# Optimization experiments

Hardware: AMD Instinct MI355X
Metric: run time of the kernel (lower is better)

Reference implementation:

```python
import jax, jax.numpy as jnp
import numpy as np

B, T, E = 2, 2048, 1024
H, D = 16, 64          # num_heads, head_dim (v_head_dim == head_dim)


def setup_inputs() -> dict:
    key = jax.random.key(0)
    ks = jax.random.split(key, 10)
    s = lambda fan_in: 1.0 / np.sqrt(fan_in)
    inp = {
        "embed": jax.random.normal(ks[0], (B, T, E), dtype=jnp.float32),
        "mask": jax.random.randint(ks[1], (B, T, T), 0, 2) > 0,
        # Linear weights stored as [in, out] (y = x @ W + b)
        "Wq": jax.random.uniform(ks[2], (E, H * D), minval=-s(E), maxval=s(E)),
        "bq": jnp.zeros((H * D,), jnp.float32),
        "Wk": jax.random.uniform(ks[3], (E, H * D), minval=-s(E), maxval=s(E)),
        "bk": jnp.zeros((H * D,), jnp.float32),
        "Wv": jax.random.uniform(ks[4], (E, H * D), minval=-s(E), maxval=s(E)),
        "bv": jnp.zeros((H * D,), jnp.float32),
        "Wz": jax.random.uniform(ks[5], (H * D, E), minval=-s(H * D), maxval=s(H * D)),
        "bz": jnp.zeros((E,), jnp.float32),
    }
    return inp


def reference(embed, mask, Wq, bq, Wk, bk, Wv, bv, Wz, bz):
    # Self-attention: context = embed
    q = (embed @ Wq + bq).reshape(B, T, H, D)   # b t h d
    k = (embed @ Wk + bk).reshape(B, T, H, D)   # b T h d
    v = (embed @ Wv + bv).reshape(B, T, H, D)   # b T h d

    scale = D ** (-0.5)
    score = jnp.einsum('bthd,bThd->bhtT', q, k) * scale   # [b,h,t,T] materialized, as in source
    max_neg = -jnp.finfo(score.dtype).max
    score = jnp.where(mask[:, None, :, :], score, max_neg)
    norm_score = jax.nn.softmax(score, axis=-1)
    z = jnp.einsum('bhtT,bThd->bthd', norm_score, v)      # [b,t,h,d]
    flat_z = z.reshape(B, T, H * D)
    return flat_z @ Wz + bz
```

## Files before the change

### kernel.cpp

```cpp
#include <hip/hip_runtime.h>
#include <hip/hip_bf16.h>


typedef __bf16 bf8_t  __attribute__((ext_vector_type(8)));
typedef __bf16 bf4_t  __attribute__((ext_vector_type(4)));
typedef float  f4_t   __attribute__((ext_vector_type(4)));

constexpr int Bb = 2, Tt = 2048, Hh = 16, Dd = 64;

#define ASYNC16(g, l)                                                        \
    __builtin_amdgcn_global_load_lds(                                        \
        (const __attribute__((address_space(1))) void*)(g),                  \
        (__attribute__((address_space(3))) void*)(l), 16, 0, 0)

#if __has_builtin(__builtin_amdgcn_exp2f)
#define EXP2F(x) __builtin_amdgcn_exp2f(x)
#else
#define EXP2F(x) exp2f(x)
#endif

__global__ __launch_bounds__(256) void prep_kernel(
    const float* __restrict__ embed, const int* __restrict__ mask,
    const float* __restrict__ w0, const float* __restrict__ w1,
    const float* __restrict__ w2, const float* __restrict__ w3,
    __bf16* __restrict__ o0, __bf16* __restrict__ o1,
    __bf16* __restrict__ o2, __bf16* __restrict__ o3,
    __bf16* __restrict__ Eb, unsigned* __restrict__ Mbits)
{
    int z = blockIdx.x;
    if (z < 4096) {
        const float* in; __bf16* out;
        switch (z >> 10) {
            case 0: in = w0; out = o0; break;
            case 1: in = w1; out = o1; break;
            case 2: in = w2; out = o2; break;
            default: in = w3; out = o3; break;
        }
        int rem = z & 1023;
        int bx = (rem & 31) * 32;
        int by = (rem >> 5) * 32;
        __shared__ float t[32][33];
        int x  = threadIdx.x & 31;
        int y0 = threadIdx.x >> 5;
        #pragma unroll
        for (int i = 0; i < 4; i++) {
            int y = y0 + i * 8;
            t[y][x] = in[(size_t)(by + y) * 1024 + bx + x];
        }
        __syncthreads();
        #pragma unroll
        for (int i = 0; i < 4; i++) {
            int y = y0 + i * 8;
            out[(size_t)(bx + y) * 1024 + by + x] = (__bf16)t[x][y];
        }
    } else if (z < 5120) {
        size_t base = (size_t)(z - 4096) * 4096;
        #pragma unroll
        for (int j = 0; j < 4; j++) {
            size_t i = base + j * 1024 + threadIdx.x * 4;
            float4 v = *reinterpret_cast<const float4*>(embed + i);
            bf4_t o = {(__bf16)v.x, (__bf16)v.y, (__bf16)v.z, (__bf16)v.w};
            *reinterpret_cast<bf4_t*>(Eb + i) = o;
        }
    } else {
        size_t g = (size_t)(z - 5120) * 256 + threadIdx.x;
        const int* mp = mask + g * 32;
        unsigned v = 0;
        #pragma unroll
        for (int i = 0; i < 8; i++) {
            int4 m4 = *reinterpret_cast<const int4*>(mp + i * 4);
            if (m4.x) v |= 1u << (i * 4 + 0);
            if (m4.y) v |= 1u << (i * 4 + 1);
            if (m4.z) v |= 1u << (i * 4 + 2);
            if (m4.w) v |= 1u << (i * 4 + 3);
        }
        Mbits[g] = v;
    }
}

template <int TM, typename OutT>
__device__ __forceinline__ void gemm_body(const __bf16* __restrict__ A,
                                          const __bf16* __restrict__ Bt,
                                          const float* __restrict__ bias,
                                          OutT* __restrict__ out,
                                          int mode, float oscale, int bx, int by)
{
    constexpr int NI = TM / 32;
    alignas(16) __shared__ __bf16 As[TM * 64];
    alignas(16) __shared__ __bf16 Bs[128 * 64];

    int tid  = threadIdx.x;
    int lane = tid & 63;
    int quad = lane >> 4;
    int l16  = lane & 15;
    int wave = tid >> 6;
    int wm   = wave >> 1, wn = wave & 1;

    f4_t acc[NI][4];
    #pragma unroll
    for (int i = 0; i < NI; i++)
        #pragma unroll
        for (int j = 0; j < 4; j++)
            acc[i][j] = f4_t{0.f, 0.f, 0.f, 0.f};

    for (int kt = 0; kt < 1024; kt += 64) {
        #pragma unroll
        for (int i = 0; i < TM / 32; i++) {
            int c   = tid + 256 * i;
            int row = c >> 3, j = c & 7;
            ASYNC16(A + (size_t)(by * TM + row) * 1024 + kt + ((j ^ (row & 7)) * 8),
                    &As[c * 8]);
        }
        #pragma unroll
        for (int i = 0; i < 4; i++) {
            int c   = tid + 256 * i;
            int row = c >> 3, j = c & 7;
            ASYNC16(Bt + (size_t)(bx * 128 + row) * 1024 + kt + ((j ^ (row & 7)) * 8),
                    &Bs[c * 8]);
        }
        __syncthreads();

        bf8_t af[2][NI], bfr[2][4];
        #pragma unroll
        for (int c = 0; c < 2; c++) {
            #pragma unroll
            for (int im = 0; im < NI; im++) {
                int row = wm * (TM / 2) + im * 16 + l16;
                af[c][im] = *reinterpret_cast<const bf8_t*>(
                    &As[row * 64 + (((c * 4 + quad) ^ (row & 7)) * 8)]);
            }
            #pragma unroll
            for (int in_ = 0; in_ < 4; in_++) {
                int row = wn * 64 + in_ * 16 + l16;
                bfr[c][in_] = *reinterpret_cast<const bf8_t*>(
                    &Bs[row * 64 + (((c * 4 + quad) ^ (row & 7)) * 8)]);
            }
        }
        #pragma unroll
        for (int c = 0; c < 2; c++)
            #pragma unroll
            for (int im = 0; im < NI; im++)
                #pragma unroll
                for (int in_ = 0; in_ < 4; in_++)
                    acc[im][in_] = __builtin_amdgcn_mfma_f32_16x16x32_bf16(
                        af[c][im], bfr[c][in_], acc[im][in_], 0, 0, 0);
        __syncthreads();
    }

    #pragma unroll
    for (int im = 0; im < NI; im++) {
        #pragma unroll
        for (int in_ = 0; in_ < 4; in_++) {
            int gc  = bx * 128 + wn * 64 + in_ * 16 + l16;
            float bb = bias[gc];
            int gr0 = by * TM + wm * (TM / 2) + im * 16 + quad * 4;
            if (mode == 2) {
                int b = gr0 >> 11, t0 = gr0 & 2047;
                int h = gc >> 6,  d = gc & 63;
                bf4_t ov;
                #pragma unroll
                for (int r = 0; r < 4; r++)
                    ov[r] = (__bf16)(acc[im][in_][r] + bb);
                *reinterpret_cast<bf4_t*>(
                    (__bf16*)out + ((size_t)(b * Hh + h) * Dd + d) * Tt + t0) = ov;
            } else {
                #pragma unroll
                for (int r = 0; r < 4; r++) {
                    int gr  = gr0 + r;
                    float v = (acc[im][in_][r] + bb) * oscale;
                    size_t idx;
                    if (mode == 0) {
                        idx = (size_t)gr * 1024 + gc;
                    } else {
                        int b = gr >> 11, t = gr & 2047;
                        int h = gc >> 6,  d = gc & 63;
                        idx = ((size_t)(b * Hh + h) * Tt + t) * Dd + d;
                    }
                    out[idx] = (OutT)v;
                }
            }
        }
    }
}

__global__ __launch_bounds__(256) void gemm_qkv_kernel(
    const __bf16* __restrict__ A,
    const __bf16* __restrict__ WqT, const __bf16* __restrict__ WkT, const __bf16* __restrict__ WvT,
    const float* __restrict__ bq,  const float* __restrict__ bk,  const float* __restrict__ bv,
    __bf16* __restrict__ Qo, __bf16* __restrict__ Ko, __bf16* __restrict__ Vo)
{
    const __bf16* Bt; const float* bias; __bf16* out; int mode; float sc;
    if      (blockIdx.z == 0) { Bt = WqT; bias = bq; out = Qo; mode = 1; sc = 0.18033688011112042f; }
    else if (blockIdx.z == 1) { Bt = WkT; bias = bk; out = Ko; mode = 1; sc = 1.f; }
    else                      { Bt = WvT; bias = bv; out = Vo; mode = 2; sc = 1.f; }
    gemm_body<128, __bf16>(A, Bt, bias, out, mode, sc, blockIdx.x, blockIdx.y);
}

__global__ __launch_bounds__(256) void gemm_out_kernel(
    const __bf16* __restrict__ A, const __bf16* __restrict__ Bt,
    const float* __restrict__ bias, float* __restrict__ out)
{
    gemm_body<64, float>(A, Bt, bias, out, 0, 1.f, blockIdx.x, blockIdx.y);
}

__global__ __launch_bounds__(1024, 8) void flash_kernel(
    const __bf16* __restrict__ Qb, const __bf16* __restrict__ Kb,
    const __bf16* __restrict__ Vb, const unsigned* __restrict__ Mbits,
    __bf16* __restrict__ Zb)
{
    alignas(16) __shared__ char smem[51200];
    __bf16* Ks = (__bf16*)smem;
    __bf16* Vs = (__bf16*)(smem + 16384);
    __bf16* Ps = (__bf16*)(smem + 32768);
    float*  fscr = (float*)smem;

    int tid  = threadIdx.x;
    int lane = tid & 63;
    int wave = tid >> 6;
    int s    = wave >> 1;
    int hk   = wave & 1;
    int quad = lane >> 4;
    int l16  = lane & 15;
    int b = blockIdx.z, h = blockIdx.y;
    int bh = b * Hh + h;
    int qrow = blockIdx.x * 128 + s * 16;

    int st = tid & 511, srow = st >> 3, sj = st & 7;
    bool stageK = (wave < 8);
    const __bf16* kgp = Kb + ((size_t)bh * Tt + srow) * Dd + ((sj ^ (srow & 7)) * 8);
    const __bf16* vgp = Vb + ((size_t)bh * Dd + srow) * Tt + ((sj ^ (srow & 7)) * 8);
    const __bf16* sgp = stageK ? kgp : vgp;
    const size_t  sstep = stageK ? (size_t)64 * Dd : (size_t)64;
    __bf16* sdstp = (stageK ? Ks : Vs) + st * 8;

    bf8_t qf[2];
    #pragma unroll
    for (int c = 0; c < 2; c++)
        qf[c] = *reinterpret_cast<const bf8_t*>(
            Qb + ((size_t)bh * Tt + qrow + l16) * Dd + c * 32 + quad * 8);

    bf8_t ones;
    #pragma unroll
    for (int i = 0; i < 8; i++) ones[i] = (__bf16)1.0f;

    const unsigned* bmp = Mbits + ((size_t)b * Tt + qrow + l16) * 64;

    f4_t lacc = f4_t{0.f, 0.f, 0.f, 0.f};
    f4_t o[4];
    #pragma unroll
    for (int d = 0; d < 4; d++) o[d] = f4_t{0.f, 0.f, 0.f, 0.f};

    __bf16* pw = Ps + s * (16 * 72);

    bf8_t sreg = *reinterpret_cast<const bf8_t*>(sgp);
    unsigned long long mreg = *reinterpret_cast<const unsigned long long*>(bmp);

    for (int kt = 0; kt < Tt; kt += 64) {
        int par = (kt >> 6) & 1;
        *reinterpret_cast<bf8_t*>(sdstp + par * 4096) = sreg;
        unsigned nib0 = (unsigned)(mreg >> (hk * 32 + quad * 4)) & 0xFu;
        unsigned nib1 = (unsigned)(mreg >> (hk * 32 + 16 + quad * 4)) & 0xFu;
        __syncthreads();

        int ktn = (kt + 64 < Tt) ? kt + 64 : 0;
        sreg = *reinterpret_cast<const bf8_t*>(sgp + (size_t)(ktn >> 6) * sstep);
        mreg = *reinterpret_cast<const unsigned long long*>(bmp + (ktn >> 5));

        f4_t sA = f4_t{0.f, 0.f, 0.f, 0.f};
        f4_t sB = f4_t{0.f, 0.f, 0.f, 0.f};
        __builtin_amdgcn_s_setprio(1);
        #pragma unroll
        for (int c = 0; c < 2; c++) {
            int krow0 = hk * 32 + l16;
            bf8_t kf0 = *reinterpret_cast<const bf8_t*>(
                &Ks[par * 4096 + krow0 * 64 + (((c * 4 + quad) ^ (krow0 & 7)) * 8)]);
            sA = __builtin_amdgcn_mfma_f32_16x16x32_bf16(kf0, qf[c], sA, 0, 0, 0);
            int krow1 = hk * 32 + 16 + l16;
            bf8_t kf1 = *reinterpret_cast<const bf8_t*>(
                &Ks[par * 4096 + krow1 * 64 + (((c * 4 + quad) ^ (krow1 & 7)) * 8)]);
            sB = __builtin_amdgcn_mfma_f32_16x16x32_bf16(kf1, qf[c], sB, 0, 0, 0);
        }
        __builtin_amdgcn_s_setprio(0);

        {
            bf4_t pv4;
            #pragma unroll
            for (int r = 0; r < 4; r++) {
                float p = (nib0 & (1u << r)) ? EXP2F(sA[r]) : 0.f;
                pv4[r] = (__bf16)p;
            }
            *reinterpret_cast<bf4_t*>(&pw[l16 * 72 + hk * 32 + quad * 4]) = pv4;
            #pragma unroll
            for (int r = 0; r < 4; r++) {
                float p = (nib1 & (1u << r)) ? EXP2F(sB[r]) : 0.f;
                pv4[r] = (__bf16)p;
            }
            *reinterpret_cast<bf4_t*>(&pw[l16 * 72 + hk * 32 + 16 + quad * 4]) = pv4;
        }

        bf8_t pf = *reinterpret_cast<const bf8_t*>(
            &pw[l16 * 72 + hk * 32 + quad * 8]);
        __builtin_amdgcn_s_setprio(1);
        lacc = __builtin_amdgcn_mfma_f32_16x16x32_bf16(ones, pf, lacc, 0, 0, 0);
        #pragma unroll
        for (int ds = 0; ds < 4; ds++) {
            int vrow = ds * 16 + l16;
            bf8_t vf = *reinterpret_cast<const bf8_t*>(
                &Vs[par * 4096 + vrow * 64 + (((hk * 4 + quad) ^ (vrow & 7)) * 8)]);
            o[ds] = __builtin_amdgcn_mfma_f32_16x16x32_bf16(vf, pf, o[ds], 0, 0, 0);
        }
        __builtin_amdgcn_s_setprio(0);
    }

    __syncthreads();
    float* ws = fscr + s * (64 * 20);
    if (hk) {
        #pragma unroll
        for (int ds = 0; ds < 4; ds++)
            *reinterpret_cast<f4_t*>(&ws[lane * 20 + ds * 4]) = o[ds];
        ws[lane * 20 + 16] = lacc[0];
    }
    __syncthreads();
    if (!hk) {
        #pragma unroll
        for (int ds = 0; ds < 4; ds++) {
            f4_t op = *reinterpret_cast<const f4_t*>(&ws[lane * 20 + ds * 4]);
            o[ds] += op;
        }
        float l = lacc[0] + ws[lane * 20 + 16];
        float inv = 1.f / fmaxf(l, 1e-30f);
        size_t zrow = ((size_t)b * Tt + qrow + l16) * 1024 + h * 64;
        #pragma unroll
        for (int ds = 0; ds < 4; ds++) {
            bf4_t ov;
            #pragma unroll
            for (int r = 0; r < 4; r++) ov[r] = (__bf16)(o[ds][r] * inv);
            *reinterpret_cast<bf4_t*>(Zb + zrow + ds * 16 + quad * 4) = ov;
        }
    }
}

extern "C" void kernel_launch(void* const* d_in, const int* in_sizes, int n_in,
                              void* d_out, int out_size, void* d_ws, size_t ws_size,
                              hipStream_t stream)
{
    (void)in_sizes; (void)n_in; (void)out_size; (void)ws_size;

    const float* embed = (const float*)d_in[0];
    const int*   mask  = (const int*)d_in[1];
    const float* Wq = (const float*)d_in[2];
    const float* bq = (const float*)d_in[3];
    const float* Wk = (const float*)d_in[4];
    const float* bk = (const float*)d_in[5];
    const float* Wv = (const float*)d_in[6];
    const float* bv = (const float*)d_in[7];
    const float* Wz = (const float*)d_in[8];
    const float* bz = (const float*)d_in[9];
    float* out = (float*)d_out;

    char* ws = (char*)d_ws;
    const size_t MB = (size_t)1024 * 1024;
    __bf16*   WqT = (__bf16*)(ws + 0 * MB);
    __bf16*   WkT = (__bf16*)(ws + 2 * MB);
    __bf16*   WvT = (__bf16*)(ws + 4 * MB);
    __bf16*   WzT = (__bf16*)(ws + 6 * MB);
    __bf16*   Eb  = (__bf16*)(ws + 8 * MB);
    __bf16*   Qb  = (__bf16*)(ws + 16 * MB);
    __bf16*   Kb  = (__bf16*)(ws + 24 * MB);
    __bf16*   Vb  = (__bf16*)(ws + 32 * MB);
    __bf16*   Zb  = (__bf16*)(ws + 40 * MB);
    unsigned* Mb  = (unsigned*)(ws + 48 * MB);

    prep_kernel<<<dim3(6144), 256, 0, stream>>>(embed, mask, Wq, Wk, Wv, Wz,
                                                WqT, WkT, WvT, WzT, Eb, Mb);
    gemm_qkv_kernel<<<dim3(8, 32, 3), 256, 0, stream>>>(Eb, WqT, WkT, WvT,
                                                        bq, bk, bv, Qb, Kb, Vb);
    flash_kernel<<<dim3(16, Hh, Bb), 1024, 0, stream>>>(Qb, Kb, Vb, Mb, Zb);
    gemm_out_kernel<<<dim3(8, 64, 1), 256, 0, stream>>>(Zb, WzT, bz, out);
}
```

Baseline: 235.4 us.

## Halve flash attention block size and swizzle the P scratch layout

The flash kernel now runs 512-thread blocks covering 64 query rows instead of 1024-thread blocks covering 128, and the grid doubles to keep the same total work. Each thread now stages both a K and a V vector per tile, and shared memory drops to 40 KB. The P tile scratch moves from a padded 72-element stride to a 128-byte row with an XOR swizzle, meant to avoid LDS bank conflicts. This aims at better occupancy and scheduling flexibility, at the cost of each K/V tile being reloaded by twice as many blocks.

```diff
diff --git a/kernel.cpp b/kernel.cpp
--- a/kernel.cpp
+++ b/kernel.cpp
@@ -203,15 +203,15 @@
     gemm_body<64, float>(A, Bt, bias, out, 0, 1.f, blockIdx.x, blockIdx.y);
 }
 
-__global__ __launch_bounds__(1024, 8) void flash_kernel(
+__global__ __launch_bounds__(512, 8) void flash_kernel(
     const __bf16* __restrict__ Qb, const __bf16* __restrict__ Kb,
     const __bf16* __restrict__ Vb, const unsigned* __restrict__ Mbits,
     __bf16* __restrict__ Zb)
 {
-    alignas(16) __shared__ char smem[51200];
-    __bf16* Ks = (__bf16*)smem;
-    __bf16* Vs = (__bf16*)(smem + 16384);
-    __bf16* Ps = (__bf16*)(smem + 32768);
+    alignas(16) __shared__ char smem[40960];
+    __bf16* Ks  = (__bf16*)smem;
+    __bf16* Vs  = (__bf16*)(smem + 16384);
+    char*   Pb  = smem + 32768;
     float*  fscr = (float*)smem;
 
     int tid  = threadIdx.x;
@@ -223,15 +223,12 @@
     int l16  = lane & 15;
     int b = blockIdx.z, h = blockIdx.y;
     int bh = b * Hh + h;
-    int qrow = blockIdx.x * 128 + s * 16;
-
-    int st = tid & 511, srow = st >> 3, sj = st & 7;
-    bool stageK = (wave < 8);
+    int qrow = blockIdx.x * 64 + s * 16;
+
+    int srow = tid >> 3, sj = tid & 7;
     const __bf16* kgp = Kb + ((size_t)bh * Tt + srow) * Dd + ((sj ^ (srow & 7)) * 8);
     const __bf16* vgp = Vb + ((size_t)bh * Dd + srow) * Tt + ((sj ^ (srow & 7)) * 8);
-    const __bf16* sgp = stageK ? kgp : vgp;
-    const size_t  sstep = stageK ? (size_t)64 * Dd : (size_t)64;
-    __bf16* sdstp = (stageK ? Ks : Vs) + st * 8;
+    const int sdst = tid * 8;
 
     bf8_t qf[2];
     #pragma unroll
@@ -245,25 +242,31 @@
 
     const unsigned* bmp = Mbits + ((size_t)b * Tt + qrow + l16) * 64;
 
+    char* pws = Pb + s * 2048;
+    const int pw0 = l16 * 128 + ((hk * 64 + quad * 8)      ^ ((l16 & 7) << 4));
+    const int pw1 = l16 * 128 + ((hk * 64 + 32 + quad * 8) ^ ((l16 & 7) << 4));
+    const int prd = l16 * 128 + ((hk * 64 + quad * 16)     ^ ((l16 & 7) << 4));
+
     f4_t lacc = f4_t{0.f, 0.f, 0.f, 0.f};
     f4_t o[4];
     #pragma unroll
     for (int d = 0; d < 4; d++) o[d] = f4_t{0.f, 0.f, 0.f, 0.f};
 
-    __bf16* pw = Ps + s * (16 * 72);
-
-    bf8_t sreg = *reinterpret_cast<const bf8_t*>(sgp);
+    bf8_t kreg = *reinterpret_cast<const bf8_t*>(kgp);
+    bf8_t vreg = *reinterpret_cast<const bf8_t*>(vgp);
     unsigned long long mreg = *reinterpret_cast<const unsigned long long*>(bmp);
 
     for (int kt = 0; kt < Tt; kt += 64) {
         int par = (kt >> 6) & 1;
-        *reinterpret_cast<bf8_t*>(sdstp + par * 4096) = sreg;
+        *reinterpret_cast<bf8_t*>(&Ks[par * 4096 + sdst]) = kreg;
+        *reinterpret_cast<bf8_t*>(&Vs[par * 4096 + sdst]) = vreg;
         unsigned nib0 = (unsigned)(mreg >> (hk * 32 + quad * 4)) & 0xFu;
         unsigned nib1 = (unsigned)(mreg >> (hk * 32 + 16 + quad * 4)) & 0xFu;
         __syncthreads();
 
         int ktn = (kt + 64 < Tt) ? kt + 64 : 0;
-        sreg = *reinterpret_cast<const bf8_t*>(sgp + (size_t)(ktn >> 6) * sstep);
+        kreg = *reinterpret_cast<const bf8_t*>(kgp + (size_t)ktn * Dd);
+        vreg = *reinterpret_cast<const bf8_t*>(vgp + ktn);
         mreg = *reinterpret_cast<const unsigned long long*>(bmp + (ktn >> 5));
 
         f4_t sA = f4_t{0.f, 0.f, 0.f, 0.f};
@@ -289,17 +292,16 @@
                 float p = (nib0 & (1u << r)) ? EXP2F(sA[r]) : 0.f;
                 pv4[r] = (__bf16)p;
             }
-            *reinterpret_cast<bf4_t*>(&pw[l16 * 72 + hk * 32 + quad * 4]) = pv4;
+            *reinterpret_cast<bf4_t*>(pws + pw0) = pv4;
             #pragma unroll
             for (int r = 0; r < 4; r++) {
                 float p = (nib1 & (1u << r)) ? EXP2F(sB[r]) : 0.f;
                 pv4[r] = (__bf16)p;
             }
-            *reinterpret_cast<bf4_t*>(&pw[l16 * 72 + hk * 32 + 16 + quad * 4]) = pv4;
-        }
-
-        bf8_t pf = *reinterpret_cast<const bf8_t*>(
-            &pw[l16 * 72 + hk * 32 + quad * 8]);
+            *reinterpret_cast<bf4_t*>(pws + pw1) = pv4;
+        }
+
+        bf8_t pf = *reinterpret_cast<const bf8_t*>(pws + prd);
         __builtin_amdgcn_s_setprio(1);
         lacc = __builtin_amdgcn_mfma_f32_16x16x32_bf16(ones, pf, lacc, 0, 0, 0);
         #pragma unroll
@@ -313,21 +315,21 @@
     }
 
     __syncthreads();
-    float* ws = fscr + s * (64 * 20);
+    float* wsp = fscr + s * (64 * 20);
     if (hk) {
         #pragma unroll
         for (int ds = 0; ds < 4; ds++)
-            *reinterpret_cast<f4_t*>(&ws[lane * 20 + ds * 4]) = o[ds];
-        ws[lane * 20 + 16] = lacc[0];
+            *reinterpret_cast<f4_t*>(&wsp[lane * 20 + ds * 4]) = o[ds];
+        wsp[lane * 20 + 16] = lacc[0];
     }
     __syncthreads();
     if (!hk) {
         #pragma unroll
         for (int ds = 0; ds < 4; ds++) {
-            f4_t op = *reinterpret_cast<const f4_t*>(&ws[lane * 20 + ds * 4]);
+            f4_t op = *reinterpret_cast<const f4_t*>(&wsp[lane * 20 + ds * 4]);
             o[ds] += op;
         }
-        float l = lacc[0] + ws[lane * 20 + 16];
+        float l = lacc[0] + wsp[lane * 20 + 16];
         float inv = 1.f / fmaxf(l, 1e-30f);
         size_t zrow = ((size_t)b * Tt + qrow + l16) * 1024 + h * 64;
         #pragma unroll
@@ -375,6 +377,6 @@
                                                 WqT, WkT, WvT, WzT, Eb, Mb);
     gemm_qkv_kernel<<<dim3(8, 32, 3), 256, 0, stream>>>(Eb, WqT, WkT, WvT,
                                                         bq, bk, bv, Qb, Kb, Vb);
-    flash_kernel<<<dim3(16, Hh, Bb), 1024, 0, stream>>>(Qb, Kb, Vb, Mb, Zb);
+    flash_kernel<<<dim3(32, Hh, Bb), 512, 0, stream>>>(Qb, Kb, Vb, Mb, Zb);
     gemm_out_kernel<<<dim3(8, 64, 1), 256, 0, stream>>>(Zb, WzT, bz, out);
 }
```

Result: slower. 282.2 us (+19.9%).
